# Kernel tuning notes

Hardware: AMD Instinct MI355X
Metric: run time of the kernel (lower is better)

## Reference

```python
import jax, jax.numpy as jnp
import numpy as np

N, E, B, H, L = 50000, 500000, 64, 64, 4


def setup_inputs() -> dict:
    key = jax.random.key(0)
    ks = jax.random.split(key, 32)
    def w(k, shp, fan_in):
        s = 1.0 / np.sqrt(fan_in)
        return jax.random.uniform(k, shp, jnp.float32, -s, s)
    inp = {
        "v0": jax.random.normal(ks[0], (N, 1), jnp.float32),
        "v1": jax.random.normal(ks[1], (N, 1), jnp.float32),
        "dist": jax.random.uniform(ks[2], (E, 1), jnp.float32),
        "edge_index": jax.random.randint(ks[3], (2, E), 0, N, jnp.int32),
        "batch": jnp.sort(jax.random.randint(ks[4], (N,), 0, B, jnp.int32)),
        "batch_size": B,
        # embeddings / per-input linears
        "wte": jax.random.normal(ks[5], (2, H), jnp.float32),
        "W_in0": w(ks[6], (H, 1), 1), "b_in0": w(ks[7], (H,), 1),
        "W_in1": w(ks[8], (H, 1), 1), "b_in1": w(ks[9], (H,), 1),
        "W_out0": w(ks[10], (1, H), H), "b_out0": w(ks[11], (1,), H),
        "W_out1": w(ks[12], (1, H), H), "b_out1": w(ks[13], (1,), H),
        "W_edge": w(ks[14], (H, 1), 1), "b_edge": w(ks[15], (H,), 1),
        # shared GraphBlock (ModuleList([block]*L) shares weights)
        "W_el": w(ks[16], (H, 2 * H), 2 * H), "b_el": w(ks[17], (H,), 2 * H),
        "W_n1": w(ks[18], (4 * H, 3 * H), 3 * H), "b_n1": w(ks[19], (4 * H,), 3 * H),
        "W_n2": w(ks[20], (H, 4 * H), 4 * H), "b_n2": w(ks[21], (H,), 4 * H),
        "W_gl": w(ks[22], (H, 2 * H), 2 * H), "b_gl": w(ks[23], (H,), 2 * H),
        # shared LSTMCell
        "W_ih": w(ks[24], (4 * H, H), H), "W_hh": w(ks[25], (4 * H, H), H),
        "b_ih": w(ks[26], (4 * H,), H), "b_hh": w(ks[27], (4 * H,), H),
    }
    return inp


def _forward(v0, v1, dist, edge_index, batch, batch_size,
             wte, W_in0, b_in0, W_in1, b_in1, W_out0, b_out0, W_out1, b_out1,
             W_edge, b_edge, W_el, b_el, W_n1, b_n1, W_n2, b_n2, W_gl, b_gl,
             W_ih, W_hh, b_ih, b_hh):
    # x = sum_i (type_embedding_i + Linear_i(v_i))  -> [N, H]
    x = (wte[0] + v0 @ W_in0.T + b_in0) + (wte[1] + v1 @ W_in1.T + b_in1)
    e = dist @ W_edge.T + b_edge                      # [E, H]
    u = jnp.zeros((batch_size, x.shape[-1]), x.dtype)  # [B, H]
    row, col = edge_index[0], edge_index[1]
    n_nodes = x.shape[0]
    cs = []
    for _ in range(L):  # shared weights across layers (faithful to [block]*L)
        # edge MLP on gathered source features, scatter-max to destination nodes
        msg = jax.nn.relu(jnp.concatenate([x[row], e], axis=-1) @ W_el.T + b_el)
        agg = jax.ops.segment_max(msg, col, num_segments=n_nodes)
        agg = jnp.where(jnp.isfinite(agg), agg, 0.0)  # empty segments -> 0
        # node MLP with residual
        h1 = jax.nn.relu(jnp.concatenate([agg, x, u[batch]], axis=-1) @ W_n1.T + b_n1)
        x = x + h1 @ W_n2.T + b_n2
        # global update: per-graph max over nodes
        x_u = jax.ops.segment_max(x, batch, num_segments=batch_size)
        x_u = jnp.where(jnp.isfinite(x_u), x_u, 0.0)
        u = u + jax.nn.relu(jnp.concatenate([x_u, u], axis=-1) @ W_gl.T + b_gl)
        # LSTMCell with zero initial (h, c) every layer (hidden_states=None path)
        gates = u @ W_ih.T + b_ih + b_hh  # h_prev = 0 so W_hh term vanishes
        i_g, f_g, g_g, o_g = jnp.split(gates, 4, axis=-1)
        c = jax.nn.sigmoid(i_g) * jnp.tanh(g_g)        # c_prev = 0
        u = jax.nn.sigmoid(o_g) * jnp.tanh(c)
        cs.append(c)
    outs = jnp.stack([x @ W_out0.T + b_out0, x @ W_out1.T + b_out1])  # [2, N, 1]
    return outs, jnp.stack(cs)  # ([2,N,1], [L,B,H])


def reference(v0, v1, dist, edge_index, batch, batch_size,
              wte, W_in0, b_in0, W_in1, b_in1, W_out0, b_out0, W_out1, b_out1,
              W_edge, b_edge, W_el, b_el, W_n1, b_n1, W_n2, b_n2, W_gl, b_gl,
              W_ih, W_hh, b_ih, b_hh):
    return _forward(v0, v1, dist, edge_index, batch, batch_size,
                    wte, W_in0, b_in0, W_in1, b_in1, W_out0, b_out0, W_out1, b_out1,
                    W_edge, b_edge, W_el, b_el, W_n1, b_n1, W_n2, b_n2, W_gl, b_gl,
                    W_ih, W_hh, b_ih, b_hh)
```

## Files before the change

kernel.cpp:

```cpp
#include <hip/hip_runtime.h>


typedef __attribute__((ext_vector_type(8))) short short8;
typedef __attribute__((ext_vector_type(4))) float f32x4;

__device__ __forceinline__ unsigned short f2bf(float f) {
  union { float f; unsigned u; } v; v.f = f;
  unsigned r = v.u + 0x7FFFu + ((v.u >> 16) & 1u);
  return (unsigned short)(r >> 16);
}
__device__ __forceinline__ float bf2f(unsigned short s) {
  return __uint_as_float((unsigned)s << 16);
}
__device__ __forceinline__ unsigned enc_ordered(float f) {
  unsigned u = __float_as_uint(f);
  return (u >> 31) ? ~u : (u | 0x80000000u);
}

__global__ void k_init(const float* __restrict__ v0, const float* __restrict__ v1,
                       const float* __restrict__ wte,
                       const float* __restrict__ Wi0, const float* __restrict__ bi0,
                       const float* __restrict__ Wi1, const float* __restrict__ bi1,
                       const int* __restrict__ batch,
                       int* __restrict__ gstart, int* __restrict__ gend,
                       float* __restrict__ x,
                       float* __restrict__ u, unsigned* __restrict__ xu_enc,
                       unsigned short* __restrict__ W1b, unsigned short* __restrict__ W2b,
                       unsigned short* __restrict__ Welb,
                       const float* __restrict__ W_n1, const float* __restrict__ W_n2,
                       const float* __restrict__ W_el,
                       const float* __restrict__ b_el,
                       const float* __restrict__ W_edge, const float* __restrict__ b_edge,
                       float* __restrict__ p, float* __restrict__ q,
                       float* __restrict__ c0, float* __restrict__ c1,
                       float* __restrict__ c2,
                       int* __restrict__ deg, int* __restrict__ cur, int N) {
  int gt = blockIdx.x * 256 + threadIdx.x;
  int NH = N * 64;
  if (gt < NH) {
    int n = gt >> 6, h = gt & 63;
    x[gt] = wte[h] + wte[64 + h] + bi0[h] + bi1[h] + v0[n] * Wi0[h] + v1[n] * Wi1[h];
    if (h == 0) {
      int bg = batch[n];
      if (n == 0 || batch[n - 1] != bg) gstart[bg] = n;
      if (n == N - 1 || batch[n + 1] != bg) gend[bg] = n + 1;
    }
    return;
  }
  int i = gt - NH;
  if (i < 4096) {
    u[i] = 0.f;
  } else if (i < 8192) {
    xu_enc[i - 4096] = 0x007FFFFFu;
  } else if (i < 8192 + 49152) {
    int j = i - 8192;
    W1b[j] = f2bf(W_n1[j]);
  } else if (i < 8192 + 49152 + 16384) {
    int j = i - 57344;
    W2b[j] = f2bf(W_n2[j]);
  } else if (i < 77824) {
    int j = i - 73728;
    Welb[j] = f2bf(W_el[(j >> 6) * 128 + (j & 63)]);
  } else if (i < 77824 + N) {
    deg[i - 77824] = 0;
  } else if (i < 77824 + 2 * N) {
    cur[i - 77824 - N] = 0;
  } else if (i < 77824 + 2 * N + 64) {
    int h = i - 77824 - 2 * N;
    float pp = 0.f, qq = 0.f, s0 = 0.f, s1 = 0.f, s2 = 0.f;
    for (int k = 0; k < 64; ++k) {
      float w2 = W_el[h * 128 + 64 + k];
      pp += w2 * W_edge[k];
      qq += w2 * b_edge[k];
      float w1 = W_el[h * 128 + k];
      float base = wte[k] + wte[64 + k] + bi0[k] + bi1[k];
      s0 += w1 * base;
      s1 += w1 * Wi0[k];
      s2 += w1 * Wi1[k];
    }
    p[h] = pp; q[h] = qq + b_el[h];
    c0[h] = s0; c1[h] = s1; c2[h] = s2;
  }
}

__global__ __launch_bounds__(256) void k_hist(const int* __restrict__ eidx,
                                              int* __restrict__ deg, int E) {
  int e = blockIdx.x * 256 + threadIdx.x;
  if (e < E) atomicAdd(&deg[eidx[E + e]], 1);
}

__global__ __launch_bounds__(256) void k_scan1(const int* __restrict__ deg,
                                               int* __restrict__ off,
                                               int* __restrict__ bsum, int N) {
  __shared__ int s[256];
  int b = blockIdx.x, t = threadIdx.x;
  int i0 = b * 512 + t * 2;
  int v0 = (i0 < N) ? deg[i0] : 0;
  int v1 = (i0 + 1 < N) ? deg[i0 + 1] : 0;
  int sum = v0 + v1;
  s[t] = sum;
  __syncthreads();
  for (int d = 1; d < 256; d <<= 1) {
    int val = (t >= d) ? s[t - d] : 0;
    __syncthreads();
    s[t] += val;
    __syncthreads();
  }
  int excl = s[t] - sum;
  if (i0 < N) off[i0] = excl + v0;
  if (i0 + 1 < N) off[i0 + 1] = excl + v0 + v1;
  if (t == 255) bsum[b] = s[t];
}

__global__ void k_scan2(int* __restrict__ bsum, int nb) {
  __shared__ int s[128];
  int t = threadIdx.x;
  int v = (t < nb) ? bsum[t] : 0;
  s[t] = v;
  __syncthreads();
  for (int d = 1; d < 128; d <<= 1) {
    int val = (t >= d) ? s[t - d] : 0;
    __syncthreads();
    s[t] += val;
    __syncthreads();
  }
  if (t < nb) bsum[t] = s[t] - v;
}

__global__ __launch_bounds__(256) void k_scatter(const int* __restrict__ eidx,
                                                 const float* __restrict__ dist,
                                                 const int* __restrict__ off,
                                                 const int* __restrict__ bsum,
                                                 int* __restrict__ cur,
                                                 uint2* __restrict__ spack, int E) {
  int e = blockIdx.x * 256 + threadIdx.x;
  if (e >= E) return;
  int c = eidx[E + e];
  int base = (c == 0) ? 0 : (off[c - 1] + bsum[(c - 1) >> 9]);
  int pos = base + atomicAdd(&cur[c], 1);
  spack[pos] = make_uint2((unsigned)eidx[e] | ((unsigned)(c & 31) << 27),
                          __float_as_uint(dist[e]));
}

template <int MODE>
__global__ __launch_bounds__(256) void k_node(
    const int* __restrict__ off, const int* __restrict__ bsum,
    const uint2* __restrict__ spack,
    const float* __restrict__ p, const float* __restrict__ q,
    const float* __restrict__ c0, const float* __restrict__ c1,
    const float* __restrict__ c2,
    const float* __restrict__ v0, const float* __restrict__ v1,
    float* __restrict__ x, unsigned short* __restrict__ y_bf,
    const int* __restrict__ batch, const float* __restrict__ u,
    const unsigned short* __restrict__ W1b, const unsigned short* __restrict__ W2b,
    const unsigned short* __restrict__ Welb,
    const float* __restrict__ b_n1, const float* __restrict__ b_n2,
    unsigned* __restrict__ xu_enc,
    float* __restrict__ bmaxA, float* __restrict__ bmaxB,
    int* __restrict__ bgidA, int* __restrict__ bgidB,
    const float* __restrict__ Wo0, const float* __restrict__ bo0,
    const float* __restrict__ Wo1, const float* __restrict__ bo1,
    float* __restrict__ outp, int N) {
  __shared__ __align__(16) char inb[32 * 384];
  __shared__ __align__(16) char h1T[32 * 512];
  __shared__ uint2 smeta[256];
  __shared__ int sgb[32];
  int t = threadIdx.x;
  int n0 = blockIdx.x * 32;
  int lane = t & 63, wv = t >> 6;
  int lr = lane & 15;
  int lk8 = (lane >> 4) << 3;
  int jo = (lane >> 4) << 2;
  int swzr = (lr & 7) << 4;
  int h0 = wv * 16 + jo;

  float4 xo[2];
#pragma unroll
  for (int nt = 0; nt < 2; ++nt) {
    int node = n0 + nt * 16 + lr;
    xo[nt] = (node < N) ? *(const float4*)(x + (size_t)node * 64 + h0)
                        : make_float4(0.f, 0.f, 0.f, 0.f);
  }
  int nd_s = t >> 3, ko = t & 7;
  int node_s = n0 + nd_s;
  float4 ua = make_float4(0.f, 0.f, 0.f, 0.f), ub = ua;
  if (node_s < N) {
    int g = batch[node_s];
    const float4* u4 = (const float4*)u;
    ua = u4[g * 16 + ko * 2];
    ub = u4[g * 16 + ko * 2 + 1];
  }
  if (t < 32) sgb[t] = batch[min(n0 + t, N - 1)];

  int* aggi = (int*)h1T;
#pragma unroll
  for (int i = 0; i < 8; ++i) aggi[t + i * 256] = 0;

#pragma unroll
  for (int nt = 0; nt < 2; ++nt) {
    int nd = nt * 16 + lr;
    unsigned lo = (unsigned)f2bf(xo[nt].x) | ((unsigned)f2bf(xo[nt].y) << 16);
    unsigned hi = (unsigned)f2bf(xo[nt].z) | ((unsigned)f2bf(xo[nt].w) << 16);
    *(uint2*)(inb + nd * 384 + ((128 + h0 * 2) ^ ((nd & 7) << 4))) = make_uint2(lo, hi);
  }
  {
    int swz = (nd_s & 7) << 4;
    uint4 uv;
    uv.x = f2bf(ua.x) | ((unsigned)f2bf(ua.y) << 16);
    uv.y = f2bf(ua.z) | ((unsigned)f2bf(ua.w) << 16);
    uv.z = f2bf(ub.x) | ((unsigned)f2bf(ub.y) << 16);
    uv.w = f2bf(ub.z) | ((unsigned)f2bf(ub.w) << 16);
    *(uint4*)(inb + nd_s * 384 + ((256 + ko * 16) ^ swz)) = uv;
  }
  __syncthreads();

  {
    int last = min(n0 + 31, N - 1);
    int ebase = (n0 == 0) ? 0 : (off[n0 - 1] + bsum[(n0 - 1) >> 9]);
    int eend = off[last] + bsum[last >> 9];
    int total = eend - ebase;
    int q4 = total >> 2;
    int wb = ebase + wv * q4;
    int we = (wv == 3) ? eend : (wb + q4);
    uint2* sm = smeta + wv * 64;
    int half = lane >> 5, l31 = lane & 31;
    const unsigned* y32 = (const unsigned*)y_bf + l31;
    float2 p2 = *(const float2*)(p + 2 * l31);
    float2 q2 = *(const float2*)(q + 2 * l31);
    float2 c02 = make_float2(0.f, 0.f), c12 = c02, c22 = c02;
    if (MODE == 0) {
      c02 = *(const float2*)(c0 + 2 * l31);
      c12 = *(const float2*)(c1 + 2 * l31);
      c22 = *(const float2*)(c2 + 2 * l31);
    }
    float m0 = 0.f, m1 = 0.f;
    int ccur = -1;
    uint2 r = make_uint2(0u, 0u);
    if (wb < we) {
      int cnt = min(64, we - wb);
      if (lane < cnt) r = spack[wb + lane];
    }
    for (int cb = wb; cb < we; cb += 64) {
      int ccnt = min(64, we - cb);
      sm[lane] = r;
      int nb = cb + 64;
      if (nb < we) {
        int ncnt = we - nb;
        if (lane < ncnt) r = spack[nb + lane];
      }
      int nfull = ccnt >> 1;
      int i = 0;
      for (; i + 8 <= nfull; i += 8) {
        uint2 e[8]; unsigned yd[8]; float va[8], vb[8];
#pragma unroll
        for (int k = 0; k < 8; ++k) e[k] = sm[2 * (i + k) + half];
#pragma unroll
        for (int k = 0; k < 8; ++k) {
          unsigned row = e[k].x & 0x07FFFFFFu;
          if (MODE == 0) { va[k] = v0[row]; vb[k] = v1[row]; }
          else yd[k] = y32[row << 5];
        }
#pragma unroll
        for (int k = 0; k < 8; ++k) {
          float y0f, y1f;
          if (MODE == 0) {
            y0f = fmaf(vb[k], c22.x, fmaf(va[k], c12.x, c02.x));
            y1f = fmaf(vb[k], c22.y, fmaf(va[k], c12.y, c02.y));
          } else {
            y0f = __uint_as_float(yd[k] << 16);
            y1f = __uint_as_float(yd[k] & 0xFFFF0000u);
          }
          float d = __uint_as_float(e[k].y);
          float g0 = fmaxf(fmaf(d, p2.x, y0f + q2.x), 0.f);
          float g1 = fmaxf(fmaf(d, p2.y, y1f + q2.y), 0.f);
          int c = (int)(e[k].x >> 27);
          if (c != ccur) {
            if (ccur >= 0) {
              atomicMax(&aggi[ccur * 64 + 2 * l31], __float_as_int(m0));
              atomicMax(&aggi[ccur * 64 + 2 * l31 + 1], __float_as_int(m1));
            }
            ccur = c; m0 = g0; m1 = g1;
          } else { m0 = fmaxf(m0, g0); m1 = fmaxf(m1, g1); }
        }
      }
      for (; 2 * i < ccnt; ++i) {
        int idx = 2 * i + half;
        bool val = idx < ccnt;
        uint2 e = sm[val ? idx : 0];
        unsigned row = e.x & 0x07FFFFFFu;
        float y0f, y1f;
        if (MODE == 0) {
          float a = v0[row], b = v1[row];
          y0f = fmaf(b, c22.x, fmaf(a, c12.x, c02.x));
          y1f = fmaf(b, c22.y, fmaf(a, c12.y, c02.y));
        } else {
          unsigned yd = y32[row << 5];
          y0f = __uint_as_float(yd << 16);
          y1f = __uint_as_float(yd & 0xFFFF0000u);
        }
        float d = __uint_as_float(e.y);
        float g0 = val ? fmaxf(fmaf(d, p2.x, y0f + q2.x), 0.f) : 0.f;
        float g1 = val ? fmaxf(fmaf(d, p2.y, y1f + q2.y), 0.f) : 0.f;
        int c = val ? (int)(e.x >> 27) : ccur;
        if (c != ccur) {
          if (ccur >= 0) {
            atomicMax(&aggi[ccur * 64 + 2 * l31], __float_as_int(m0));
            atomicMax(&aggi[ccur * 64 + 2 * l31 + 1], __float_as_int(m1));
          }
          ccur = c; m0 = g0; m1 = g1;
        } else { m0 = fmaxf(m0, g0); m1 = fmaxf(m1, g1); }
      }
    }
    if (ccur >= 0) {
      atomicMax(&aggi[ccur * 64 + 2 * l31], __float_as_int(m0));
      atomicMax(&aggi[ccur * 64 + 2 * l31 + 1], __float_as_int(m1));
    }
  }
  __syncthreads();

  {
    int swz = (nd_s & 7) << 4;
    const float4* ag4 = (const float4*)(h1T);
    float4 aa = ag4[nd_s * 16 + ko * 2];
    float4 ab = ag4[nd_s * 16 + ko * 2 + 1];
    uint4 av;
    av.x = f2bf(aa.x) | ((unsigned)f2bf(aa.y) << 16);
    av.y = f2bf(aa.z) | ((unsigned)f2bf(aa.w) << 16);
    av.z = f2bf(ab.x) | ((unsigned)f2bf(ab.y) << 16);
    av.w = f2bf(ab.z) | ((unsigned)f2bf(ab.w) << 16);
    *(uint4*)(inb + nd_s * 384 + ((ko * 16) ^ swz)) = av;
  }
  __syncthreads();

  int w = wv;

  f32x4 acc[4][2];
#pragma unroll
  for (int ot = 0; ot < 4; ++ot)
#pragma unroll
    for (int nt = 0; nt < 2; ++nt) acc[ot][nt] = (f32x4){0.f, 0.f, 0.f, 0.f};
  const unsigned short* W1p = W1b + (w * 64 + lr) * 192 + lk8;
#pragma unroll
  for (int ks = 0; ks < 6; ++ks) {
    int kb = ks * 64 + lk8 * 2;
    short8 b0 = *(const short8*)(inb + lr * 384 + (kb ^ swzr));
    short8 b1 = *(const short8*)(inb + (16 + lr) * 384 + (kb ^ swzr));
#pragma unroll
    for (int ot = 0; ot < 4; ++ot) {
      short8 a = *(const short8*)(W1p + ot * (16 * 192) + ks * 32);
      acc[ot][0] = __builtin_amdgcn_mfma_f32_16x16x32_bf16(a, b0, acc[ot][0], 0, 0, 0);
      acc[ot][1] = __builtin_amdgcn_mfma_f32_16x16x32_bf16(a, b1, acc[ot][1], 0, 0, 0);
    }
  }
  __syncthreads();
#pragma unroll
  for (int ot = 0; ot < 4; ++ot) {
    int o = w * 64 + ot * 16 + jo;
    float4 bs = *(const float4*)(b_n1 + o);
#pragma unroll
    for (int nt = 0; nt < 2; ++nt) {
      int nd = nt * 16 + lr;
      unsigned lo = (unsigned)f2bf(fmaxf(acc[ot][nt][0] + bs.x, 0.f)) |
                    ((unsigned)f2bf(fmaxf(acc[ot][nt][1] + bs.y, 0.f)) << 16);
      unsigned hi = (unsigned)f2bf(fmaxf(acc[ot][nt][2] + bs.z, 0.f)) |
                    ((unsigned)f2bf(fmaxf(acc[ot][nt][3] + bs.w, 0.f)) << 16);
      *(uint2*)(h1T + nd * 512 + ((o * 2) ^ ((nd & 7) << 4))) = make_uint2(lo, hi);
    }
  }
  __syncthreads();

  f32x4 acc2[2] = {{0.f, 0.f, 0.f, 0.f}, {0.f, 0.f, 0.f, 0.f}};
  const unsigned short* W2p = W2b + (w * 16 + lr) * 256 + lk8;
#pragma unroll
  for (int ks = 0; ks < 8; ++ks) {
    short8 a = *(const short8*)(W2p + ks * 32);
    int kb = ks * 64 + lk8 * 2;
    short8 b0 = *(const short8*)(h1T + lr * 512 + (kb ^ swzr));
    short8 b1 = *(const short8*)(h1T + (16 + lr) * 512 + (kb ^ swzr));
    acc2[0] = __builtin_amdgcn_mfma_f32_16x16x32_bf16(a, b0, acc2[0], 0, 0, 0);
    acc2[1] = __builtin_amdgcn_mfma_f32_16x16x32_bf16(a, b1, acc2[1], 0, 0, 0);
  }
  float4 b2 = *(const float4*)(b_n2 + h0);
  char* xnb = inb;
  float4 xn[2];
#pragma unroll
  for (int nt = 0; nt < 2; ++nt) {
    int nd = nt * 16 + lr;
    int node = n0 + nd;
    xn[nt].x = xo[nt].x + acc2[nt][0] + b2.x;
    xn[nt].y = xo[nt].y + acc2[nt][1] + b2.y;
    xn[nt].z = xo[nt].z + acc2[nt][2] + b2.z;
    xn[nt].w = xo[nt].w + acc2[nt][3] + b2.w;
    if (node >= N) xn[nt] = make_float4(0.f, 0.f, 0.f, 0.f);
    if (MODE != 2 && node < N) *(float4*)(x + (size_t)node * 64 + h0) = xn[nt];
    if (MODE != 2) {
      unsigned lo = (unsigned)f2bf(xn[nt].x) | ((unsigned)f2bf(xn[nt].y) << 16);
      unsigned hi = (unsigned)f2bf(xn[nt].z) | ((unsigned)f2bf(xn[nt].w) << 16);
      *(uint2*)(xnb + nd * 128 + ((h0 * 2) ^ ((nd & 7) << 4))) = make_uint2(lo, hi);
    }
  }

  {
    const float NEG = -__builtin_huge_valf();
    int gA = sgb[0], gB = sgb[31];
    float a0 = NEG, a1 = NEG, a2 = NEG, a3 = NEG;
    float e0 = NEG, e1 = NEG, e2 = NEG, e3 = NEG;
#pragma unroll
    for (int nt = 0; nt < 2; ++nt) {
      int nd = nt * 16 + lr;
      if (n0 + nd < N) {
        int g = sgb[nd];
        if (g == gA) {
          a0 = fmaxf(a0, xn[nt].x); a1 = fmaxf(a1, xn[nt].y);
          a2 = fmaxf(a2, xn[nt].z); a3 = fmaxf(a3, xn[nt].w);
        } else if (g == gB) {
          e0 = fmaxf(e0, xn[nt].x); e1 = fmaxf(e1, xn[nt].y);
          e2 = fmaxf(e2, xn[nt].z); e3 = fmaxf(e3, xn[nt].w);
        } else {
          unsigned* xe = xu_enc + g * 64 + h0;
          atomicMax(xe + 0, enc_ordered(xn[nt].x));
          atomicMax(xe + 1, enc_ordered(xn[nt].y));
          atomicMax(xe + 2, enc_ordered(xn[nt].z));
          atomicMax(xe + 3, enc_ordered(xn[nt].w));
        }
      }
    }
#pragma unroll
    for (int msk = 1; msk <= 8; msk <<= 1) {
      a0 = fmaxf(a0, __shfl_xor(a0, msk)); a1 = fmaxf(a1, __shfl_xor(a1, msk));
      a2 = fmaxf(a2, __shfl_xor(a2, msk)); a3 = fmaxf(a3, __shfl_xor(a3, msk));
      e0 = fmaxf(e0, __shfl_xor(e0, msk)); e1 = fmaxf(e1, __shfl_xor(e1, msk));
      e2 = fmaxf(e2, __shfl_xor(e2, msk)); e3 = fmaxf(e3, __shfl_xor(e3, msk));
    }
    if (lr == 0) {
      size_t base = (size_t)blockIdx.x * 64 + h0;
      bmaxA[base + 0] = a0; bmaxA[base + 1] = a1;
      bmaxA[base + 2] = a2; bmaxA[base + 3] = a3;
      bmaxB[base + 0] = e0; bmaxB[base + 1] = e1;
      bmaxB[base + 2] = e2; bmaxB[base + 3] = e3;
    }
    if (t == 0) {
      bgidA[blockIdx.x] = gA;
      bgidB[blockIdx.x] = (gB == gA) ? -1 : gB;
    }
  }
  __syncthreads();

  if (MODE != 2) {
    f32x4 acc3[2] = {{0.f, 0.f, 0.f, 0.f}, {0.f, 0.f, 0.f, 0.f}};
    const unsigned short* W3p = Welb + (w * 16 + lr) * 64 + lk8;
#pragma unroll
    for (int ks = 0; ks < 2; ++ks) {
      short8 a = *(const short8*)(W3p + ks * 32);
      int kb = ks * 64 + lk8 * 2;
      short8 b0 = *(const short8*)(xnb + lr * 128 + (kb ^ swzr));
      short8 b1 = *(const short8*)(xnb + (16 + lr) * 128 + (kb ^ swzr));
      acc3[0] = __builtin_amdgcn_mfma_f32_16x16x32_bf16(a, b0, acc3[0], 0, 0, 0);
      acc3[1] = __builtin_amdgcn_mfma_f32_16x16x32_bf16(a, b1, acc3[1], 0, 0, 0);
    }
    int o0 = w * 16 + jo;
#pragma unroll
    for (int nt = 0; nt < 2; ++nt) {
      int node = n0 + nt * 16 + lr;
      if (node < N) {
        unsigned lo = (unsigned)f2bf(acc3[nt][0]) | ((unsigned)f2bf(acc3[nt][1]) << 16);
        unsigned hi = (unsigned)f2bf(acc3[nt][2]) | ((unsigned)f2bf(acc3[nt][3]) << 16);
        *(uint2*)(y_bf + (size_t)node * 64 + o0) = make_uint2(lo, hi);
      }
    }
  } else {
    float4 w0 = *(const float4*)(Wo0 + h0);
    float4 w1 = *(const float4*)(Wo1 + h0);
    float* ow = (float*)h1T;
#pragma unroll
    for (int nt = 0; nt < 2; ++nt) {
      float p0 = xn[nt].x * w0.x + xn[nt].y * w0.y + xn[nt].z * w0.z + xn[nt].w * w0.w;
      float p1 = xn[nt].x * w1.x + xn[nt].y * w1.y + xn[nt].z * w1.z + xn[nt].w * w1.w;
      p0 += __shfl_xor(p0, 16); p0 += __shfl_xor(p0, 32);
      p1 += __shfl_xor(p1, 16); p1 += __shfl_xor(p1, 32);
      if (lane < 16) {
        ow[w * 64 + 0 + nt * 16 + lr] = p0;
        ow[w * 64 + 32 + nt * 16 + lr] = p1;
      }
    }
    __syncthreads();
    if (t < 64) {
      int oi = t >> 5, nd = t & 31;
      int node = n0 + nd;
      if (node < N) {
        float v = ow[0 * 64 + oi * 32 + nd] + ow[1 * 64 + oi * 32 + nd] +
                  ow[2 * 64 + oi * 32 + nd] + ow[3 * 64 + oi * 32 + nd];
        v += (oi ? bo1[0] : bo0[0]);
        outp[(size_t)oi * N + node] = v;
      }
    }
  }
}

__global__ __launch_bounds__(256) void k_graph(const int* __restrict__ gstart,
                                               const int* __restrict__ gend,
                                               const float* __restrict__ bmaxA,
                                               const float* __restrict__ bmaxB,
                                               const int* __restrict__ bgidA,
                                               const int* __restrict__ bgidB,
                                               unsigned* __restrict__ xu_enc,
                                               float* __restrict__ u,
                                               const float* __restrict__ W_gl,
                                               const float* __restrict__ b_gl,
                                               const float* __restrict__ W_ih,
                                               const float* __restrict__ b_ih,
                                               const float* __restrict__ b_hh,
                                               float* __restrict__ c_out) {
  __shared__ float red[4][3][64];
  __shared__ float xu_s[64], us[64], un[64];
  int g = blockIdx.x;
  int t = threadIdx.x, h = t & 63, qd = t >> 6;
  const float NEG = -__builtin_huge_valf();

  float m = NEG;
  int gs = gstart[g], ge = gend[g];
  if (gs < ge) {
    int bs = gs >> 5, be = (ge - 1) >> 5;
    for (int b = bs + qd; b <= be; b += 4) {
      if (bgidA[b] == g) m = fmaxf(m, bmaxA[(size_t)b * 64 + h]);
      if (bgidB[b] == g) m = fmaxf(m, bmaxB[(size_t)b * 64 + h]);
    }
  }
  red[qd][0][h] = m;
  __syncthreads();
  if (qd == 0) {
    m = fmaxf(fmaxf(red[0][0][h], red[1][0][h]), fmaxf(red[2][0][h], red[3][0][h]));
    unsigned Ev = xu_enc[g * 64 + h];
    float fd = (Ev & 0x80000000u) ? __uint_as_float(Ev & 0x7FFFFFFFu)
                                  : __uint_as_float(~Ev);
    m = fmaxf(m, fd);
    xu_enc[g * 64 + h] = 0x007FFFFFu;
    xu_s[h] = isfinite(m) ? m : 0.f;
    us[h] = u[g * 64 + h];
  }
  __syncthreads();

  float pre = 0.f;
  {
    const float* Wrow = W_gl + h * 128 + qd * 32;
    const float* src = (qd < 2) ? (xu_s + qd * 32) : (us + (qd - 2) * 32);
#pragma unroll 8
    for (int k = 0; k < 32; ++k) pre += src[k] * Wrow[k];
  }
  red[qd][0][h] = pre;
  __syncthreads();
  if (qd == 0) {
    float prs = red[0][0][h] + red[1][0][h] + red[2][0][h] + red[3][0][h] + b_gl[h];
    un[h] = us[h] + fmaxf(prs, 0.f);
  }
  __syncthreads();

  float gi = 0.f, gg = 0.f, go = 0.f;
#pragma unroll 4
  for (int k = qd * 16; k < qd * 16 + 16; ++k) {
    float uv = un[k];
    gi += uv * W_ih[h * 64 + k];
    gg += uv * W_ih[(128 + h) * 64 + k];
    go += uv * W_ih[(192 + h) * 64 + k];
  }
  red[qd][0][h] = gi; red[qd][1][h] = gg; red[qd][2][h] = go;
  __syncthreads();
  if (qd == 0) {
    gi = red[0][0][h] + red[1][0][h] + red[2][0][h] + red[3][0][h] + b_ih[h] + b_hh[h];
    gg = red[0][1][h] + red[1][1][h] + red[2][1][h] + red[3][1][h] +
         b_ih[128 + h] + b_hh[128 + h];
    go = red[0][2][h] + red[1][2][h] + red[2][2][h] + red[3][2][h] +
         b_ih[192 + h] + b_hh[192 + h];
    float cc = (1.f / (1.f + expf(-gi))) * tanhf(gg);
    float u2v = (1.f / (1.f + expf(-go))) * tanhf(cc);
    c_out[g * 64 + h] = cc;
    u[g * 64 + h] = u2v;
  }
}

extern "C" void kernel_launch(void* const* d_in, const int* in_sizes, int n_in,
                              void* d_out, int out_size, void* d_ws, size_t ws_size,
                              hipStream_t stream) {
  const float* v0 = (const float*)d_in[0];
  const float* v1 = (const float*)d_in[1];
  const float* dist = (const float*)d_in[2];
  const int* eidx = (const int*)d_in[3];
  const int* batch = (const int*)d_in[4];
  const float* wte = (const float*)d_in[6];
  const float* Wi0 = (const float*)d_in[7];
  const float* bi0 = (const float*)d_in[8];
  const float* Wi1 = (const float*)d_in[9];
  const float* bi1 = (const float*)d_in[10];
  const float* Wo0 = (const float*)d_in[11];
  const float* bo0 = (const float*)d_in[12];
  const float* Wo1 = (const float*)d_in[13];
  const float* bo1 = (const float*)d_in[14];
  const float* W_edge = (const float*)d_in[15];
  const float* b_edge = (const float*)d_in[16];
  const float* W_el = (const float*)d_in[17];
  const float* b_el = (const float*)d_in[18];
  const float* W_n1 = (const float*)d_in[19];
  const float* b_n1 = (const float*)d_in[20];
  const float* W_n2 = (const float*)d_in[21];
  const float* b_n2 = (const float*)d_in[22];
  const float* W_gl = (const float*)d_in[23];
  const float* b_gl = (const float*)d_in[24];
  const float* W_ih = (const float*)d_in[25];
  const float* b_ih = (const float*)d_in[27];
  const float* b_hh = (const float*)d_in[28];

  const int N = in_sizes[0];
  const int E = in_sizes[2];
  const int NH = N * 64;
  const int NB512 = (N + 511) / 512;
  const int nblk = (N + 31) / 32;

  float* ws = (float*)d_ws;
  float* x = ws;
  float* u = x + NH;
  unsigned* xu_enc = (unsigned*)(u + 4096);
  float* p = (float*)(xu_enc + 4096);
  float* q = p + 64;
  float* c0 = q + 64;
  float* c1 = c0 + 64;
  float* c2 = c1 + 64;
  unsigned short* W1b = (unsigned short*)(c2 + 64);
  unsigned short* W2b = W1b + 49152;
  unsigned short* Welb = W2b + 16384;
  unsigned short* y_bf = Welb + 4096;
  int* deg = (int*)(y_bf + NH);
  int* off = deg + N;
  int* cur = off + N;
  int* bsum = cur + N;
  int* gstart = bsum + 128;
  int* gend = gstart + 64;
  int* bgidA = gend + 64;
  int* bgidB = bgidA + nblk;
  float* bmaxA = (float*)(bgidB + nblk);
  float* bmaxB = bmaxA + (size_t)nblk * 64;
  uint2* spack = (uint2*)(((size_t)(bmaxB + (size_t)nblk * 64) + 15) & ~(size_t)15);

  float* outp = (float*)d_out;

  k_init<<<(NH + 77824 + 2 * N + 64 + 255) / 256, 256, 0, stream>>>(
      v0, v1, wte, Wi0, bi0, Wi1, bi1, batch, gstart, gend, x,
      u, xu_enc, W1b, W2b, Welb, W_n1, W_n2, W_el, b_el, W_edge, b_edge,
      p, q, c0, c1, c2, deg, cur, N);
  k_hist<<<(E + 255) / 256, 256, 0, stream>>>(eidx, deg, E);
  k_scan1<<<NB512, 256, 0, stream>>>(deg, off, bsum, N);
  k_scan2<<<1, 128, 0, stream>>>(bsum, NB512);
  k_scatter<<<(E + 255) / 256, 256, 0, stream>>>(eidx, dist, off, bsum, cur, spack, E);

  for (int l = 0; l < 4; ++l) {
    if (l == 0) {
      k_node<0><<<nblk, 256, 0, stream>>>(off, bsum, spack, p, q, c0, c1, c2, v0, v1,
                                          x, y_bf, batch, u, W1b, W2b, Welb, b_n1, b_n2,
                                          xu_enc, bmaxA, bmaxB, bgidA, bgidB,
                                          Wo0, bo0, Wo1, bo1, outp, N);
    } else if (l < 3) {
      k_node<1><<<nblk, 256, 0, stream>>>(off, bsum, spack, p, q, c0, c1, c2, v0, v1,
                                          x, y_bf, batch, u, W1b, W2b, Welb, b_n1, b_n2,
                                          xu_enc, bmaxA, bmaxB, bgidA, bgidB,
                                          Wo0, bo0, Wo1, bo1, outp, N);
    } else {
      k_node<2><<<nblk, 256, 0, stream>>>(off, bsum, spack, p, q, c0, c1, c2, v0, v1,
                                          x, y_bf, batch, u, W1b, W2b, Welb, b_n1, b_n2,
                                          xu_enc, bmaxA, bmaxB, bgidA, bgidB,
                                          Wo0, bo0, Wo1, bo1, outp, N);
    }
    k_graph<<<64, 256, 0, stream>>>(gstart, gend, bmaxA, bmaxB, bgidA, bgidB,
                                    xu_enc, u, W_gl, b_gl, W_ih, b_ih, b_hh,
                                    outp + 2 * N + l * 4096);
  }
}
```

Before: 313.9 us.

## Compute initial node features inline and regroup edge gather into 16-lane groups

Layer 0 now computes the initial node embedding x on the fly from v0/v1 and the input-linear weights, so the init kernel no longer writes the full N×64 x array. The gstart/gend detection moves to a per-node thread range. The edge aggregation loop is rewritten so each 16-lane group walks its own contiguous chunk of edges, and each lane handles 4 hidden channels with 8-byte bf16 loads. This drops the shared-memory staging of edge metadata and the half-wave split. The trade-off is more uncoalesced per-lane spack loads and more atomics per flush, in exchange for fewer passes and wider gathers.

```diff
diff --git a/kernel.cpp b/kernel.cpp
--- a/kernel.cpp
+++ b/kernel.cpp
@@ -23,7 +23,6 @@
                        const float* __restrict__ Wi1, const float* __restrict__ bi1,
                        const int* __restrict__ batch,
                        int* __restrict__ gstart, int* __restrict__ gend,
-                       float* __restrict__ x,
                        float* __restrict__ u, unsigned* __restrict__ xu_enc,
                        unsigned short* __restrict__ W1b, unsigned short* __restrict__ W2b,
                        unsigned short* __restrict__ Welb,
@@ -35,19 +34,7 @@
                        float* __restrict__ c0, float* __restrict__ c1,
                        float* __restrict__ c2,
                        int* __restrict__ deg, int* __restrict__ cur, int N) {
-  int gt = blockIdx.x * 256 + threadIdx.x;
-  int NH = N * 64;
-  if (gt < NH) {
-    int n = gt >> 6, h = gt & 63;
-    x[gt] = wte[h] + wte[64 + h] + bi0[h] + bi1[h] + v0[n] * Wi0[h] + v1[n] * Wi1[h];
-    if (h == 0) {
-      int bg = batch[n];
-      if (n == 0 || batch[n - 1] != bg) gstart[bg] = n;
-      if (n == N - 1 || batch[n + 1] != bg) gend[bg] = n + 1;
-    }
-    return;
-  }
-  int i = gt - NH;
+  int i = blockIdx.x * 256 + threadIdx.x;
   if (i < 4096) {
     u[i] = 0.f;
   } else if (i < 8192) {
@@ -65,8 +52,13 @@
     deg[i - 77824] = 0;
   } else if (i < 77824 + 2 * N) {
     cur[i - 77824 - N] = 0;
-  } else if (i < 77824 + 2 * N + 64) {
-    int h = i - 77824 - 2 * N;
+  } else if (i < 77824 + 3 * N) {
+    int n = i - 77824 - 2 * N;
+    int bg = batch[n];
+    if (n == 0 || batch[n - 1] != bg) gstart[bg] = n;
+    if (n == N - 1 || batch[n + 1] != bg) gend[bg] = n + 1;
+  } else if (i < 77824 + 3 * N + 64) {
+    int h = i - 77824 - 3 * N;
     float pp = 0.f, qq = 0.f, s0 = 0.f, s1 = 0.f, s2 = 0.f;
     for (int k = 0; k < 64; ++k) {
       float w2 = W_el[h * 128 + 64 + k];
@@ -150,6 +142,9 @@
     const float* __restrict__ c0, const float* __restrict__ c1,
     const float* __restrict__ c2,
     const float* __restrict__ v0, const float* __restrict__ v1,
+    const float* __restrict__ wte,
+    const float* __restrict__ Wi0, const float* __restrict__ bi0,
+    const float* __restrict__ Wi1, const float* __restrict__ bi1,
     float* __restrict__ x, unsigned short* __restrict__ y_bf,
     const int* __restrict__ batch, const float* __restrict__ u,
     const unsigned short* __restrict__ W1b, const unsigned short* __restrict__ W2b,
@@ -163,7 +158,6 @@
     float* __restrict__ outp, int N) {
   __shared__ __align__(16) char inb[32 * 384];
   __shared__ __align__(16) char h1T[32 * 512];
-  __shared__ uint2 smeta[256];
   __shared__ int sgb[32];
   int t = threadIdx.x;
   int n0 = blockIdx.x * 32;
@@ -175,11 +169,32 @@
   int h0 = wv * 16 + jo;
 
   float4 xo[2];
-#pragma unroll
-  for (int nt = 0; nt < 2; ++nt) {
-    int node = n0 + nt * 16 + lr;
-    xo[nt] = (node < N) ? *(const float4*)(x + (size_t)node * 64 + h0)
-                        : make_float4(0.f, 0.f, 0.f, 0.f);
+  if (MODE == 0) {
+    float4 wA = *(const float4*)(wte + h0);
+    float4 wB = *(const float4*)(wte + 64 + h0);
+    float4 bA = *(const float4*)(bi0 + h0);
+    float4 bB = *(const float4*)(bi1 + h0);
+    float4 w0v = *(const float4*)(Wi0 + h0);
+    float4 w1v = *(const float4*)(Wi1 + h0);
+    float4 cb = make_float4(wA.x + wB.x + bA.x + bB.x, wA.y + wB.y + bA.y + bB.y,
+                            wA.z + wB.z + bA.z + bB.z, wA.w + wB.w + bA.w + bB.w);
+#pragma unroll
+    for (int nt = 0; nt < 2; ++nt) {
+      int node = n0 + nt * 16 + lr;
+      float a = (node < N) ? v0[node] : 0.f;
+      float b = (node < N) ? v1[node] : 0.f;
+      xo[nt].x = cb.x + a * w0v.x + b * w1v.x;
+      xo[nt].y = cb.y + a * w0v.y + b * w1v.y;
+      xo[nt].z = cb.z + a * w0v.z + b * w1v.z;
+      xo[nt].w = cb.w + a * w0v.w + b * w1v.w;
+    }
+  } else {
+#pragma unroll
+    for (int nt = 0; nt < 2; ++nt) {
+      int node = n0 + nt * 16 + lr;
+      xo[nt] = (node < N) ? *(const float4*)(x + (size_t)node * 64 + h0)
+                          : make_float4(0.f, 0.f, 0.f, 0.f);
+    }
   }
   int nd_s = t >> 3, ko = t & 7;
   int node_s = n0 + nd_s;
@@ -219,102 +234,105 @@
     int ebase = (n0 == 0) ? 0 : (off[n0 - 1] + bsum[(n0 - 1) >> 9]);
     int eend = off[last] + bsum[last >> 9];
     int total = eend - ebase;
-    int q4 = total >> 2;
-    int wb = ebase + wv * q4;
-    int we = (wv == 3) ? eend : (wb + q4);
-    uint2* sm = smeta + wv * 64;
-    int half = lane >> 5, l31 = lane & 31;
-    const unsigned* y32 = (const unsigned*)y_bf + l31;
-    float2 p2 = *(const float2*)(p + 2 * l31);
-    float2 q2 = *(const float2*)(q + 2 * l31);
-    float2 c02 = make_float2(0.f, 0.f), c12 = c02, c22 = c02;
+    int gi16 = (wv << 2) | (lane >> 4);
+    int ch = lane & 15;
+    int chunk = (total + 15) >> 4;
+    int gb = ebase + gi16 * chunk;
+    int ge = min(gb + chunk, eend);
+    const unsigned short* ybase = y_bf + ch * 4;
+    float4 p4 = *(const float4*)(p + ch * 4);
+    float4 q4 = *(const float4*)(q + ch * 4);
+    float4 c04 = make_float4(0.f, 0.f, 0.f, 0.f), c14 = c04, c24 = c04;
     if (MODE == 0) {
-      c02 = *(const float2*)(c0 + 2 * l31);
-      c12 = *(const float2*)(c1 + 2 * l31);
-      c22 = *(const float2*)(c2 + 2 * l31);
-    }
-    float m0 = 0.f, m1 = 0.f;
+      c04 = *(const float4*)(c0 + ch * 4);
+      c14 = *(const float4*)(c1 + ch * 4);
+      c24 = *(const float4*)(c2 + ch * 4);
+    }
+    float4 m4 = make_float4(0.f, 0.f, 0.f, 0.f);
     int ccur = -1;
-    uint2 r = make_uint2(0u, 0u);
-    if (wb < we) {
-      int cnt = min(64, we - wb);
-      if (lane < cnt) r = spack[wb + lane];
-    }
-    for (int cb = wb; cb < we; cb += 64) {
-      int ccnt = min(64, we - cb);
-      sm[lane] = r;
-      int nb = cb + 64;
-      if (nb < we) {
-        int ncnt = we - nb;
-        if (lane < ncnt) r = spack[nb + lane];
-      }
-      int nfull = ccnt >> 1;
-      int i = 0;
-      for (; i + 8 <= nfull; i += 8) {
-        uint2 e[8]; unsigned yd[8]; float va[8], vb[8];
-#pragma unroll
-        for (int k = 0; k < 8; ++k) e[k] = sm[2 * (i + k) + half];
-#pragma unroll
-        for (int k = 0; k < 8; ++k) {
-          unsigned row = e[k].x & 0x07FFFFFFu;
-          if (MODE == 0) { va[k] = v0[row]; vb[k] = v1[row]; }
-          else yd[k] = y32[row << 5];
+    int e = gb;
+#define FLUSH4()                                                            \
+  do {                                                                      \
+    atomicMax(&aggi[ccur * 64 + ch * 4 + 0], __float_as_int(m4.x));         \
+    atomicMax(&aggi[ccur * 64 + ch * 4 + 1], __float_as_int(m4.y));         \
+    atomicMax(&aggi[ccur * 64 + ch * 4 + 2], __float_as_int(m4.z));         \
+    atomicMax(&aggi[ccur * 64 + ch * 4 + 3], __float_as_int(m4.w));         \
+  } while (0)
+    for (; e + 8 <= ge; e += 8) {
+      uint2 em[8];
+#pragma unroll
+      for (int k = 0; k < 8; ++k) em[k] = spack[e + k];
+      uint2 yv[8]; float va[8], vb[8];
+#pragma unroll
+      for (int k = 0; k < 8; ++k) {
+        unsigned row = em[k].x & 0x07FFFFFFu;
+        if (MODE == 0) { va[k] = v0[row]; vb[k] = v1[row]; }
+        else yv[k] = *(const uint2*)(ybase + (size_t)row * 64);
+      }
+#pragma unroll
+      for (int k = 0; k < 8; ++k) {
+        float4 y4;
+        if (MODE == 0) {
+          y4.x = fmaf(vb[k], c24.x, fmaf(va[k], c14.x, c04.x));
+          y4.y = fmaf(vb[k], c24.y, fmaf(va[k], c14.y, c04.y));
+          y4.z = fmaf(vb[k], c24.z, fmaf(va[k], c14.z, c04.z));
+          y4.w = fmaf(vb[k], c24.w, fmaf(va[k], c14.w, c04.w));
+        } else {
+          y4.x = __uint_as_float(yv[k].x << 16);
+          y4.y = __uint_as_float(yv[k].x & 0xFFFF0000u);
+          y4.z = __uint_as_float(yv[k].y << 16);
+          y4.w = __uint_as_float(yv[k].y & 0xFFFF0000u);
         }
-#pragma unroll
-        for (int k = 0; k < 8; ++k) {
-          float y0f, y1f;
-          if (MODE == 0) {
-            y0f = fmaf(vb[k], c22.x, fmaf(va[k], c12.x, c02.x));
-            y1f = fmaf(vb[k], c22.y, fmaf(va[k], c12.y, c02.y));
-          } else {
-            y0f = __uint_as_float(yd[k] << 16);
-            y1f = __uint_as_float(yd[k] & 0xFFFF0000u);
-          }
-          float d = __uint_as_float(e[k].y);
-          float g0 = fmaxf(fmaf(d, p2.x, y0f + q2.x), 0.f);
-          float g1 = fmaxf(fmaf(d, p2.y, y1f + q2.y), 0.f);
-          int c = (int)(e[k].x >> 27);
-          if (c != ccur) {
-            if (ccur >= 0) {
-              atomicMax(&aggi[ccur * 64 + 2 * l31], __float_as_int(m0));
-              atomicMax(&aggi[ccur * 64 + 2 * l31 + 1], __float_as_int(m1));
-            }
-            ccur = c; m0 = g0; m1 = g1;
-          } else { m0 = fmaxf(m0, g0); m1 = fmaxf(m1, g1); }
+        float d = __uint_as_float(em[k].y);
+        float4 g4;
+        g4.x = fmaxf(fmaf(d, p4.x, y4.x + q4.x), 0.f);
+        g4.y = fmaxf(fmaf(d, p4.y, y4.y + q4.y), 0.f);
+        g4.z = fmaxf(fmaf(d, p4.z, y4.z + q4.z), 0.f);
+        g4.w = fmaxf(fmaf(d, p4.w, y4.w + q4.w), 0.f);
+        int c = (int)(em[k].x >> 27);
+        if (c != ccur) {
+          if (ccur >= 0) FLUSH4();
+          ccur = c; m4 = g4;
+        } else {
+          m4.x = fmaxf(m4.x, g4.x); m4.y = fmaxf(m4.y, g4.y);
+          m4.z = fmaxf(m4.z, g4.z); m4.w = fmaxf(m4.w, g4.w);
         }
       }
-      for (; 2 * i < ccnt; ++i) {
-        int idx = 2 * i + half;
-        bool val = idx < ccnt;
-        uint2 e = sm[val ? idx : 0];
-        unsigned row = e.x & 0x07FFFFFFu;
-        float y0f, y1f;
-        if (MODE == 0) {
-          float a = v0[row], b = v1[row];
-          y0f = fmaf(b, c22.x, fmaf(a, c12.x, c02.x));
-          y1f = fmaf(b, c22.y, fmaf(a, c12.y, c02.y));
-        } else {
-          unsigned yd = y32[row << 5];
-          y0f = __uint_as_float(yd << 16);
-          y1f = __uint_as_float(yd & 0xFFFF0000u);
-        }
-        float d = __uint_as_float(e.y);
-        float g0 = val ? fmaxf(fmaf(d, p2.x, y0f + q2.x), 0.f) : 0.f;
-        float g1 = val ? fmaxf(fmaf(d, p2.y, y1f + q2.y), 0.f) : 0.f;
-        int c = val ? (int)(e.x >> 27) : ccur;
-        if (c != ccur) {
-          if (ccur >= 0) {
-            atomicMax(&aggi[ccur * 64 + 2 * l31], __float_as_int(m0));
-            atomicMax(&aggi[ccur * 64 + 2 * l31 + 1], __float_as_int(m1));
-          }
-          ccur = c; m0 = g0; m1 = g1;
-        } else { m0 = fmaxf(m0, g0); m1 = fmaxf(m1, g1); }
-      }
-    }
-    if (ccur >= 0) {
-      atomicMax(&aggi[ccur * 64 + 2 * l31], __float_as_int(m0));
-      atomicMax(&aggi[ccur * 64 + 2 * l31 + 1], __float_as_int(m1));
-    }
+    }
+    for (; e < ge; ++e) {
+      uint2 em = spack[e];
+      unsigned row = em.x & 0x07FFFFFFu;
+      float4 y4;
+      if (MODE == 0) {
+        float a = v0[row], b = v1[row];
+        y4.x = fmaf(b, c24.x, fmaf(a, c14.x, c04.x));
+        y4.y = fmaf(b, c24.y, fmaf(a, c14.y, c04.y));
+        y4.z = fmaf(b, c24.z, fmaf(a, c14.z, c04.z));
+        y4.w = fmaf(b, c24.w, fmaf(a, c14.w, c04.w));
+      } else {
+        uint2 yv = *(const uint2*)(ybase + (size_t)row * 64);
+        y4.x = __uint_as_float(yv.x << 16);
+        y4.y = __uint_as_float(yv.x & 0xFFFF0000u);
+        y4.z = __uint_as_float(yv.y << 16);
+        y4.w = __uint_as_float(yv.y & 0xFFFF0000u);
+      }
+      float d = __uint_as_float(em.y);
+      float4 g4;
+      g4.x = fmaxf(fmaf(d, p4.x, y4.x + q4.x), 0.f);
+      g4.y = fmaxf(fmaf(d, p4.y, y4.y + q4.y), 0.f);
+      g4.z = fmaxf(fmaf(d, p4.z, y4.z + q4.z), 0.f);
+      g4.w = fmaxf(fmaf(d, p4.w, y4.w + q4.w), 0.f);
+      int c = (int)(em.x >> 27);
+      if (c != ccur) {
+        if (ccur >= 0) FLUSH4();
+        ccur = c; m4 = g4;
+      } else {
+        m4.x = fmaxf(m4.x, g4.x); m4.y = fmaxf(m4.y, g4.y);
+        m4.z = fmaxf(m4.z, g4.z); m4.w = fmaxf(m4.w, g4.w);
+      }
+    }
+    if (ccur >= 0) FLUSH4();
+#undef FLUSH4
   }
   __syncthreads();
 
@@ -642,8 +660,8 @@
 
   float* outp = (float*)d_out;
 
-  k_init<<<(NH + 77824 + 2 * N + 64 + 255) / 256, 256, 0, stream>>>(
-      v0, v1, wte, Wi0, bi0, Wi1, bi1, batch, gstart, gend, x,
+  k_init<<<(77824 + 3 * N + 64 + 255) / 256, 256, 0, stream>>>(
+      v0, v1, wte, Wi0, bi0, Wi1, bi1, batch, gstart, gend,
       u, xu_enc, W1b, W2b, Welb, W_n1, W_n2, W_el, b_el, W_edge, b_edge,
       p, q, c0, c1, c2, deg, cur, N);
   k_hist<<<(E + 255) / 256, 256, 0, stream>>>(eidx, deg, E);
@@ -654,16 +672,19 @@
   for (int l = 0; l < 4; ++l) {
     if (l == 0) {
       k_node<0><<<nblk, 256, 0, stream>>>(off, bsum, spack, p, q, c0, c1, c2, v0, v1,
+                                          wte, Wi0, bi0, Wi1, bi1,
                                           x, y_bf, batch, u, W1b, W2b, Welb, b_n1, b_n2,
                                           xu_enc, bmaxA, bmaxB, bgidA, bgidB,
                                           Wo0, bo0, Wo1, bo1, outp, N);
     } else if (l < 3) {
       k_node<1><<<nblk, 256, 0, stream>>>(off, bsum, spack, p, q, c0, c1, c2, v0, v1,
+                                          wte, Wi0, bi0, Wi1, bi1,
                                           x, y_bf, batch, u, W1b, W2b, Welb, b_n1, b_n2,
                                           xu_enc, bmaxA, bmaxB, bgidA, bgidB,
                                           Wo0, bo0, Wo1, bo1, outp, N);
     } else {
       k_node<2><<<nblk, 256, 0, stream>>>(off, bsum, spack, p, q, c0, c1, c2, v0, v1,
+                                          wte, Wi0, bi0, Wi1, bi1,
                                           x, y_bf, batch, u, W1b, W2b, Welb, b_n1, b_n2,
                                           xu_enc, bmaxA, bmaxB, bgidA, bgidB,
                                           Wo0, bo0, Wo1, bo1, outp, N);
```

After: 313.2 us. About the same (-0.2%).
